# Kernel optimization log

Hardware: AMD Instinct MI355X
Metric: run time of the kernel (lower is better)

The kernel has to match this reference:

```python
import jax, jax.numpy as jnp
import numpy as np

N_DIM = 1024
HEAD_NUM = 16
HEAD_DIM = N_DIM // HEAD_NUM


def setup_inputs() -> dict:
    key = jax.random.key(0)
    ks = jax.random.split(key, 6)
    s = 1.0 / np.sqrt(N_DIM)
    return {
        "x": jax.random.normal(ks[0], (2, 2048, N_DIM), dtype=jnp.float32),
        "wq": jax.random.uniform(ks[1], (N_DIM, N_DIM), jnp.float32, -s, s),
        "wk": jax.random.uniform(ks[2], (N_DIM, N_DIM), jnp.float32, -s, s),
        "wv": jax.random.uniform(ks[3], (N_DIM, N_DIM), jnp.float32, -s, s),
        "wo": jax.random.uniform(ks[4], (N_DIM, N_DIM), jnp.float32, -s, s),
        "bo": jax.random.uniform(ks[5], (N_DIM,), jnp.float32, -s, s),
    }


def reference(x, wq, wk, wv, wo, bo):
    B, S, D = x.shape
    # torch Linear: y = x @ W.T
    def proj(w):
        return (x @ w.T).reshape(B, S, HEAD_NUM, HEAD_DIM).transpose(0, 2, 1, 3)  # [B,H,S,Dh]
    q, k, v = proj(wq), proj(wk), proj(wv)
    scale = 1.0 / np.sqrt(HEAD_DIM).astype(np.float32)
    scores = jnp.einsum("bhqd,bhkd->bhqk", q, k) * scale  # [B,H,S,S]
    attn = jax.nn.softmax(scores, axis=-1)
    y = jnp.einsum("bhqk,bhkd->bhqd", attn, v)  # [B,H,S,Dh]
    y = y.transpose(0, 2, 1, 3).reshape(B, S, D)
    return y @ wo.T + bo
```

## Files before the change

kernel.cpp:

```cpp
#include <hip/hip_runtime.h>
#include <math.h>

#define B_DIM 2
#define S_DIM 2048
#define D_DIM 1024
#define H_NUM 16
#define DH    64
#define M_DIM (B_DIM * S_DIM)

typedef __attribute__((ext_vector_type(8))) short short8;
typedef __attribute__((ext_vector_type(4))) short short4v;
typedef __attribute__((ext_vector_type(4))) float float4v;
typedef __attribute__((ext_vector_type(4))) unsigned short ushort4v;
typedef unsigned short ushort;

static __device__ __forceinline__ ushort f2bf(float f) {
    unsigned u = __float_as_uint(f);
    u += 0x7fffu + ((u >> 16) & 1u);
    return (ushort)(u >> 16);
}

static __device__ __forceinline__ float fexp2(float x) {
#if __has_builtin(__builtin_amdgcn_exp2f)
    return __builtin_amdgcn_exp2f(x);
#else
    return exp2f(x);
#endif
}

static __device__ __forceinline__ unsigned cvtpk_bf16(float lo, float hi) {
    unsigned r;
    asm("v_cvt_pk_bf16_f32 %0, %1, %2" : "=v"(r) : "v"(lo), "v"(hi));
    return r;
}

static __device__ __forceinline__ void gload_lds16(const void* g, void* l) {
    __builtin_amdgcn_global_load_lds(
        (const __attribute__((address_space(1))) void*)g,
        (__attribute__((address_space(3))) void*)l, 16, 0, 0);
}

__global__ __launch_bounds__(256)
void cast_all(const float* __restrict__ x,  const float* __restrict__ wq,
              const float* __restrict__ wk, const float* __restrict__ wv,
              const float* __restrict__ wo, ushort* __restrict__ dst)
{
    const int i = blockIdx.x * 256 + threadIdx.x;
    const float4* s;
    int off;
    if      (i < 1048576) { s = (const float4*)x;  off = 0;       }
    else if (i < 1310720) { s = (const float4*)wq; off = 1048576; }
    else if (i < 1572864) { s = (const float4*)wk; off = 1310720; }
    else if (i < 1835008) { s = (const float4*)wv; off = 1572864; }
    else                  { s = (const float4*)wo; off = 1835008; }
    const float4 v = s[i - off];
    ushort4v o;
    o[0] = f2bf(v.x); o[1] = f2bf(v.y); o[2] = f2bf(v.z); o[3] = f2bf(v.w);
    ((ushort4v*)dst)[i] = o;
}

__global__ __launch_bounds__(256)
void gemm_bf16(const ushort* __restrict__ A, const ushort* __restrict__ B,
               ushort* __restrict__ Qh, ushort* __restrict__ Kh,
               ushort* __restrict__ Vt)
{
    __shared__ ushort Asm[2][128 * 64];
    __shared__ ushort Bsm[2][128 * 64];

    const int K = 1024;
    const int NT = 16;
    const int lin = blockIdx.y * 24 + blockIdx.x;
    const int swz = (lin & 7) * 96 + (lin >> 3);
    const int n0 = (swz % 24) * 128;
    const int m0 = (swz / 24) * 128;
    const int t    = threadIdx.x;
    const int w    = t >> 6;
    const int lane = t & 63;
    const int n    = lane & 15;
    const int quad = lane >> 4;
    const int wm = w >> 1, wn = w & 1;

    const int l8 = lane >> 3;
    const int sg = (lane & 7) ^ l8;

    const int fswz[2] = { ((0 * 4 + quad) ^ (n & 7)) * 8,
                          ((1 * 4 + quad) ^ (n & 7)) * 8 };

    float4v acc[4][4];
#pragma unroll
    for (int mt = 0; mt < 4; ++mt)
#pragma unroll
        for (int nt = 0; nt < 4; ++nt) acc[mt][nt] = (float4v){0.f, 0.f, 0.f, 0.f};

#pragma unroll
    for (int i = 0; i < 4; ++i) {
        gload_lds16(&A[(size_t)(m0 + w * 32 + i * 8 + l8) * K + sg * 8],
                    &Asm[0][(w * 32 + i * 8) * 64]);
        gload_lds16(&B[(size_t)(n0 + w * 32 + i * 8 + l8) * K + sg * 8],
                    &Bsm[0][(w * 32 + i * 8) * 64]);
    }

    for (int kt6 = 0; kt6 < NT; ++kt6) {
        __syncthreads();
        const int cur = kt6 & 1;
        if (kt6 + 1 < NT) {
            const int kt1 = (kt6 + 1) * 64;
            const int nxt = cur ^ 1;
#pragma unroll
            for (int i = 0; i < 4; ++i) {
                gload_lds16(&A[(size_t)(m0 + w * 32 + i * 8 + l8) * K + kt1 + sg * 8],
                            &Asm[nxt][(w * 32 + i * 8) * 64]);
                gload_lds16(&B[(size_t)(n0 + w * 32 + i * 8 + l8) * K + kt1 + sg * 8],
                            &Bsm[nxt][(w * 32 + i * 8) * 64]);
            }
        }

        short8 af[4][2], bfr[4][2];
#pragma unroll
        for (int mt = 0; mt < 4; ++mt)
#pragma unroll
            for (int kk = 0; kk < 2; ++kk)
                af[mt][kk] = *(const short8*)&Asm[cur][(wm * 64 + mt * 16 + n) * 64 + fswz[kk]];
#pragma unroll
        for (int nt = 0; nt < 4; ++nt)
#pragma unroll
            for (int kk = 0; kk < 2; ++kk)
                bfr[nt][kk] = *(const short8*)&Bsm[cur][(wn * 64 + nt * 16 + n) * 64 + fswz[kk]];

        __builtin_amdgcn_s_setprio(1);
#pragma unroll
        for (int mt = 0; mt < 4; ++mt)
#pragma unroll
            for (int nt = 0; nt < 4; ++nt) {
                acc[mt][nt] = __builtin_amdgcn_mfma_f32_16x16x32_bf16(
                    af[mt][0], bfr[nt][0], acc[mt][nt], 0, 0, 0);
                acc[mt][nt] = __builtin_amdgcn_mfma_f32_16x16x32_bf16(
                    af[mt][1], bfr[nt][1], acc[mt][nt], 0, 0, 0);
            }
        __builtin_amdgcn_s_setprio(0);
    }

    const int wid = n0 >> 10;
    ushort* dstQK = (wid == 0) ? Qh : Kh;
    const float qs = (wid == 0) ? 0.1803368801f : 1.0f;
#pragma unroll
    for (int mt = 0; mt < 4; ++mt) {
        const int m = m0 + wm * 64 + mt * 16 + quad * 4;
        const int b = m >> 11, s = m & (S_DIM - 1);
#pragma unroll
        for (int nt = 0; nt < 4; ++nt) {
            const int ng = (n0 & 1023) + wn * 64 + nt * 16 + n;
            const int h = ng >> 6, d = ng & 63;
            const int bh = b * H_NUM + h;
            if (wid < 2) {
#pragma unroll
                for (int r = 0; r < 4; ++r)
                    dstQK[(((size_t)bh * S_DIM + s + r) << 6) + d] =
                        f2bf(acc[mt][nt][r] * qs);
            } else {
                ushort4v p;
#pragma unroll
                for (int r = 0; r < 4; ++r) p[r] = f2bf(acc[mt][nt][r]);
                *(ushort4v*)&Vt[(((size_t)bh * DH + d) << 11) + s] = p;
            }
        }
    }
}

__global__ __launch_bounds__(256)
void gemm_out(const ushort* __restrict__ A, const ushort* __restrict__ B,
              float* __restrict__ Of, const float* __restrict__ bias)
{
    __shared__ ushort Asm[2][128 * 64];
    __shared__ ushort Bsm[2][64 * 64];

    const int K = 1024;
    const int NT = 16;
    const int lin = blockIdx.y * 16 + blockIdx.x;
    const int swz = (lin & 7) * 64 + (lin >> 3);
    const int n0 = (swz % 16) * 64;
    const int m0 = (swz / 16) * 128;
    const int t    = threadIdx.x;
    const int w    = t >> 6;
    const int lane = t & 63;
    const int n    = lane & 15;
    const int quad = lane >> 4;
    const int wm = w >> 1, wn = w & 1;

    const int l8 = lane >> 3;
    const int sg = (lane & 7) ^ l8;
    const int fswz[2] = { ((0 * 4 + quad) ^ (n & 7)) * 8,
                          ((1 * 4 + quad) ^ (n & 7)) * 8 };

    float4v acc[4][2];
#pragma unroll
    for (int mt = 0; mt < 4; ++mt)
#pragma unroll
        for (int nt = 0; nt < 2; ++nt) acc[mt][nt] = (float4v){0.f, 0.f, 0.f, 0.f};

#pragma unroll
    for (int i = 0; i < 4; ++i)
        gload_lds16(&A[(size_t)(m0 + w * 32 + i * 8 + l8) * K + sg * 8],
                    &Asm[0][(w * 32 + i * 8) * 64]);
#pragma unroll
    for (int i = 0; i < 2; ++i)
        gload_lds16(&B[(size_t)(n0 + w * 16 + i * 8 + l8) * K + sg * 8],
                    &Bsm[0][(w * 16 + i * 8) * 64]);

    for (int kt6 = 0; kt6 < NT; ++kt6) {
        __syncthreads();
        const int cur = kt6 & 1;
        if (kt6 + 1 < NT) {
            const int kt1 = (kt6 + 1) * 64;
            const int nxt = cur ^ 1;
#pragma unroll
            for (int i = 0; i < 4; ++i)
                gload_lds16(&A[(size_t)(m0 + w * 32 + i * 8 + l8) * K + kt1 + sg * 8],
                            &Asm[nxt][(w * 32 + i * 8) * 64]);
#pragma unroll
            for (int i = 0; i < 2; ++i)
                gload_lds16(&B[(size_t)(n0 + w * 16 + i * 8 + l8) * K + kt1 + sg * 8],
                            &Bsm[nxt][(w * 16 + i * 8) * 64]);
        }

        short8 af[4][2], bfr[2][2];
#pragma unroll
        for (int mt = 0; mt < 4; ++mt)
#pragma unroll
            for (int kk = 0; kk < 2; ++kk)
                af[mt][kk] = *(const short8*)&Asm[cur][(wm * 64 + mt * 16 + n) * 64 + fswz[kk]];
#pragma unroll
        for (int nt = 0; nt < 2; ++nt)
#pragma unroll
            for (int kk = 0; kk < 2; ++kk)
                bfr[nt][kk] = *(const short8*)&Bsm[cur][(wn * 32 + nt * 16 + n) * 64 + fswz[kk]];

        __builtin_amdgcn_s_setprio(1);
#pragma unroll
        for (int mt = 0; mt < 4; ++mt)
#pragma unroll
            for (int nt = 0; nt < 2; ++nt) {
                acc[mt][nt] = __builtin_amdgcn_mfma_f32_16x16x32_bf16(
                    af[mt][0], bfr[nt][0], acc[mt][nt], 0, 0, 0);
                acc[mt][nt] = __builtin_amdgcn_mfma_f32_16x16x32_bf16(
                    af[mt][1], bfr[nt][1], acc[mt][nt], 0, 0, 0);
            }
        __builtin_amdgcn_s_setprio(0);
    }

#pragma unroll
    for (int mt = 0; mt < 4; ++mt) {
        const int m = m0 + wm * 64 + mt * 16 + quad * 4;
#pragma unroll
        for (int nt = 0; nt < 2; ++nt) {
            const int ng = n0 + wn * 32 + nt * 16 + n;
            const float bv = bias[ng];
#pragma unroll
            for (int r = 0; r < 4; ++r)
                Of[(size_t)(m + r) * D_DIM + ng] = acc[mt][nt][r] + bv;
        }
    }
}

__global__ __launch_bounds__(256)
void attn_mfma(const ushort* __restrict__ Qh, const ushort* __restrict__ Kh,
               const ushort* __restrict__ Vt, ushort* __restrict__ Yh)
{
    __shared__ ushort Ksm[2][64 * 64];
    __shared__ ushort Vsm[2][64 * 64];

    const int w    = threadIdx.x >> 6;
    const int lane = threadIdx.x & 63;
    const int n    = lane & 15;
    const int quad = lane >> 4;

    const int wave_id = blockIdx.x * 4 + w;
    const int bh    = wave_id >> 6;
    const int qbase = (wave_id & 63) * 32;
    const int b     = bh >> 4;
    const int h     = bh & (H_NUM - 1);

    const ushort* Qb = Qh + (((size_t)bh * S_DIM) << 6);
    const ushort* Kb = Kh + (((size_t)bh * S_DIM) << 6);
    const ushort* Vb = Vt + (((size_t)bh * DH) << 11);

    const int l8 = lane >> 3;
    const int sg = (lane & 7) ^ l8;

    short8 qa[2][2];
#pragma unroll
    for (int mt = 0; mt < 2; ++mt)
#pragma unroll
        for (int kc = 0; kc < 2; ++kc)
            qa[mt][kc] = *(const short8*)&Qb[((size_t)(qbase + mt * 16 + n) << 6) + kc * 32 + quad * 8];

    float4v O[2][4];
    float   mrow[2], lrow[2];
#pragma unroll
    for (int mt = 0; mt < 2; ++mt) {
#pragma unroll
        for (int nt = 0; nt < 4; ++nt) O[mt][nt] = (float4v){0.f, 0.f, 0.f, 0.f};
        mrow[mt] = -1e30f; lrow[mt] = 0.f;
    }

    const int fswz[2] = { ((0 * 4 + quad) ^ (n & 7)) * 8,
                          ((1 * 4 + quad) ^ (n & 7)) * 8 };
    const int h4 = (quad & 1) * 4;
    const int q2 = quad >> 1;
    int vswz[2][2];
#pragma unroll
    for (int kc = 0; kc < 2; ++kc)
#pragma unroll
        for (int cc = 0; cc < 2; ++cc)
            vswz[kc][cc] = (((4 * kc + 2 * cc + q2) ^ (n & 7)) << 3) + h4;

#pragma unroll
    for (int i = 0; i < 2; ++i) {
        gload_lds16(&Kb[(size_t)(w * 16 + i * 8 + l8) * 64 + sg * 8],
                    &Ksm[0][(w * 16 + i * 8) * 64]);
        gload_lds16(&Vb[(size_t)(w * 16 + i * 8 + l8) * 2048 + sg * 8],
                    &Vsm[0][(w * 16 + i * 8) * 64]);
    }

    for (int kb = 0; kb < S_DIM / 64; ++kb) {
        __syncthreads();
        const int cur = kb & 1;
        if (kb + 1 < S_DIM / 64) {
            const int key1 = (kb + 1) * 64;
            const int nxt  = cur ^ 1;
#pragma unroll
            for (int i = 0; i < 2; ++i) {
                gload_lds16(&Kb[(size_t)(key1 + w * 16 + i * 8 + l8) * 64 + sg * 8],
                            &Ksm[nxt][(w * 16 + i * 8) * 64]);
                gload_lds16(&Vb[(size_t)(w * 16 + i * 8 + l8) * 2048 + key1 + sg * 8],
                            &Vsm[nxt][(w * 16 + i * 8) * 64]);
            }
        }

        short8 kf[4][2];
#pragma unroll
        for (int ct = 0; ct < 4; ++ct)
#pragma unroll
            for (int kc = 0; kc < 2; ++kc)
                kf[ct][kc] = *(const short8*)&Ksm[cur][(ct * 16 + n) * 64 + fswz[kc]];

        float4v s[2][4];
        __builtin_amdgcn_s_setprio(1);
#pragma unroll
        for (int mt = 0; mt < 2; ++mt)
#pragma unroll
            for (int ct = 0; ct < 4; ++ct) {
                float4v a = (float4v){0.f, 0.f, 0.f, 0.f};
                a = __builtin_amdgcn_mfma_f32_16x16x32_bf16(kf[ct][0], qa[mt][0], a, 0, 0, 0);
                a = __builtin_amdgcn_mfma_f32_16x16x32_bf16(kf[ct][1], qa[mt][1], a, 0, 0, 0);
                s[mt][ct] = a;
            }
        __builtin_amdgcn_s_setprio(0);

        short8 vf[4][2];
#pragma unroll
        for (int nt = 0; nt < 4; ++nt) {
            const int rb = (nt * 16 + n) * 64;
#pragma unroll
            for (int kc = 0; kc < 2; ++kc) {
                const short4v g0 = *(const short4v*)&Vsm[cur][rb + vswz[kc][0]];
                const short4v g1 = *(const short4v*)&Vsm[cur][rb + vswz[kc][1]];
                vf[nt][kc] = __builtin_shufflevector(g0, g1, 0, 1, 2, 3, 4, 5, 6, 7);
            }
        }

#pragma unroll
        for (int mt = 0; mt < 2; ++mt) {
            float lm = s[mt][0][0];
#pragma unroll
            for (int ct = 0; ct < 4; ++ct)
#pragma unroll
                for (int r = 0; r < 4; ++r)
                    lm = fmaxf(lm, s[mt][ct][r]);
            lm = fmaxf(lm, __shfl_xor(lm, 16, 64));
            lm = fmaxf(lm, __shfl_xor(lm, 32, 64));

            const bool ev = lm > mrow[mt] + 8.0f;
            if (__any(ev)) {
                const float mnew  = ev ? lm : mrow[mt];
                const float alpha = fexp2(mrow[mt] - mnew);
                mrow[mt] = mnew;
                lrow[mt] *= alpha;
                const int ai = __float_as_int(alpha);
                float av[4];
#pragma unroll
                for (int r = 0; r < 4; ++r)
                    av[r] = __int_as_float(
                        __builtin_amdgcn_ds_bpermute(4 * (quad * 4 + r), ai));
#pragma unroll
                for (int nt = 0; nt < 4; ++nt)
#pragma unroll
                    for (int r = 0; r < 4; ++r) O[mt][nt][r] *= av[r];
            }

            float pv[4][4];
            float lsum = 0.f;
#pragma unroll
            for (int ct = 0; ct < 4; ++ct)
#pragma unroll
                for (int r = 0; r < 4; ++r) {
                    const float p = fexp2(s[mt][ct][r] - mrow[mt]);
                    pv[ct][r] = p;
                    lsum += p;
                }
            lrow[mt] += lsum;

            union { unsigned u[4]; short8 s8; } pk[2];
#pragma unroll
            for (int kc = 0; kc < 2; ++kc) {
                pk[kc].u[0] = cvtpk_bf16(pv[2 * kc][0],     pv[2 * kc][1]);
                pk[kc].u[1] = cvtpk_bf16(pv[2 * kc][2],     pv[2 * kc][3]);
                pk[kc].u[2] = cvtpk_bf16(pv[2 * kc + 1][0], pv[2 * kc + 1][1]);
                pk[kc].u[3] = cvtpk_bf16(pv[2 * kc + 1][2], pv[2 * kc + 1][3]);
            }

            __builtin_amdgcn_s_setprio(1);
#pragma unroll
            for (int nt = 0; nt < 4; ++nt) {
                O[mt][nt] = __builtin_amdgcn_mfma_f32_16x16x32_bf16(pk[0].s8, vf[nt][0], O[mt][nt], 0, 0, 0);
                O[mt][nt] = __builtin_amdgcn_mfma_f32_16x16x32_bf16(pk[1].s8, vf[nt][1], O[mt][nt], 0, 0, 0);
            }
            __builtin_amdgcn_s_setprio(0);
        }
    }

#pragma unroll
    for (int mt = 0; mt < 2; ++mt) {
        float ls = lrow[mt];
        ls += __shfl_xor(ls, 16, 64);
        ls += __shfl_xor(ls, 32, 64);
        const float linv = 1.f / ls;
        const int  li = __float_as_int(linv);
        float lv[4];
#pragma unroll
        for (int r = 0; r < 4; ++r)
            lv[r] = __int_as_float(
                __builtin_amdgcn_ds_bpermute(4 * (quad * 4 + r), li));
#pragma unroll
        for (int nt = 0; nt < 4; ++nt)
#pragma unroll
            for (int r = 0; r < 4; ++r) {
                const int q = qbase + mt * 16 + quad * 4 + r;
                Yh[((size_t)(b * S_DIM + q) << 10) + h * DH + nt * 16 + n] =
                    f2bf(O[mt][nt][r] * lv[r]);
            }
    }
}

extern "C" void kernel_launch(void* const* d_in, const int* in_sizes, int n_in,
                              void* d_out, int out_size, void* d_ws, size_t ws_size,
                              hipStream_t stream)
{
    const float* x  = (const float*)d_in[0];
    const float* wq = (const float*)d_in[1];
    const float* wk = (const float*)d_in[2];
    const float* wv = (const float*)d_in[3];
    const float* wo = (const float*)d_in[4];
    const float* bo = (const float*)d_in[5];
    float* out = (float*)d_out;

    const size_t MD = (size_t)M_DIM * D_DIM;
    const size_t WD = (size_t)D_DIM * D_DIM;
    ushort* xh  = (ushort*)d_ws;
    ushort* Wh  = xh + MD;
    ushort* Woh = Wh + 3 * WD;
    ushort* Qh  = Woh + WD;
    ushort* Kh  = Qh + MD;
    ushort* Vt  = Kh + MD;
    ushort* Yh  = Vt + MD;
    if (ws_size < 48u * 1024u * 1024u) return;

    dim3 blk(256);
    cast_all<<<dim3(8192), blk, 0, stream>>>(x, wq, wk, wv, wo, xh);

    gemm_bf16<<<dim3(24, 32), blk, 0, stream>>>(xh, Wh, Qh, Kh, Vt);
    attn_mfma<<<dim3(512), blk, 0, stream>>>(Qh, Kh, Vt, Yh);
    gemm_out<<<dim3(16, 32), blk, 0, stream>>>(Yh, Woh, out, bo);
}
```

Baseline: 202.8 us.

## Split attention over the key dimension with a separate merge kernel

Splits the attention key loop into two halves run as separate blocks (grid y = 2). Each half writes unnormalized fp32 partial outputs plus row max and sum to workspace, and a new merge kernel combines them with log-sum-exp rescaling into bf16 Y. The goal is more blocks in flight on the MI355X's many CUs, which the original 512-block grid leaves underused. The cost is about 32 MB of extra fp32 traffic, an additional kernel launch, and reliance on a workspace of at least 81 MB, with the old path kept as a fallback.

```diff
diff --git a/kernel.cpp b/kernel.cpp
--- a/kernel.cpp
+++ b/kernel.cpp
@@ -264,7 +264,9 @@
 
 __global__ __launch_bounds__(256)
 void attn_mfma(const ushort* __restrict__ Qh, const ushort* __restrict__ Kh,
-               const ushort* __restrict__ Vt, ushort* __restrict__ Yh)
+               const ushort* __restrict__ Vt, ushort* __restrict__ Yh,
+               float* __restrict__ Op, float* __restrict__ Lm,
+               int nkb, int partial)
 {
     __shared__ ushort Ksm[2][64 * 64];
     __shared__ ushort Vsm[2][64 * 64];
@@ -279,6 +281,8 @@
     const int qbase = (wave_id & 63) * 32;
     const int b     = bh >> 4;
     const int h     = bh & (H_NUM - 1);
+    const int s     = blockIdx.y;
+    const int kb0   = s * nkb, kb1 = kb0 + nkb;
 
     const ushort* Qb = Qh + (((size_t)bh * S_DIM) << 6);
     const ushort* Kb = Kh + (((size_t)bh * S_DIM) << 6);
@@ -314,18 +318,19 @@
         for (int cc = 0; cc < 2; ++cc)
             vswz[kc][cc] = (((4 * kc + 2 * cc + q2) ^ (n & 7)) << 3) + h4;
 
+    const int keyp = kb0 * 64;
 #pragma unroll
     for (int i = 0; i < 2; ++i) {
-        gload_lds16(&Kb[(size_t)(w * 16 + i * 8 + l8) * 64 + sg * 8],
+        gload_lds16(&Kb[(size_t)(keyp + w * 16 + i * 8 + l8) * 64 + sg * 8],
                     &Ksm[0][(w * 16 + i * 8) * 64]);
-        gload_lds16(&Vb[(size_t)(w * 16 + i * 8 + l8) * 2048 + sg * 8],
+        gload_lds16(&Vb[(size_t)(w * 16 + i * 8 + l8) * 2048 + keyp + sg * 8],
                     &Vsm[0][(w * 16 + i * 8) * 64]);
     }
 
-    for (int kb = 0; kb < S_DIM / 64; ++kb) {
+    for (int kb = kb0; kb < kb1; ++kb) {
         __syncthreads();
-        const int cur = kb & 1;
-        if (kb + 1 < S_DIM / 64) {
+        const int cur = (kb - kb0) & 1;
+        if (kb + 1 < kb1) {
             const int key1 = (kb + 1) * 64;
             const int nxt  = cur ^ 1;
 #pragma unroll
@@ -344,7 +349,7 @@
             for (int kc = 0; kc < 2; ++kc)
                 kf[ct][kc] = *(const short8*)&Ksm[cur][(ct * 16 + n) * 64 + fswz[kc]];
 
-        float4v s[2][4];
+        float4v sc[2][4];
         __builtin_amdgcn_s_setprio(1);
 #pragma unroll
         for (int mt = 0; mt < 2; ++mt)
@@ -353,7 +358,7 @@
                 float4v a = (float4v){0.f, 0.f, 0.f, 0.f};
                 a = __builtin_amdgcn_mfma_f32_16x16x32_bf16(kf[ct][0], qa[mt][0], a, 0, 0, 0);
                 a = __builtin_amdgcn_mfma_f32_16x16x32_bf16(kf[ct][1], qa[mt][1], a, 0, 0, 0);
-                s[mt][ct] = a;
+                sc[mt][ct] = a;
             }
         __builtin_amdgcn_s_setprio(0);
 
@@ -371,12 +376,12 @@
 
 #pragma unroll
         for (int mt = 0; mt < 2; ++mt) {
-            float lm = s[mt][0][0];
+            float lm = sc[mt][0][0];
 #pragma unroll
             for (int ct = 0; ct < 4; ++ct)
 #pragma unroll
                 for (int r = 0; r < 4; ++r)
-                    lm = fmaxf(lm, s[mt][ct][r]);
+                    lm = fmaxf(lm, sc[mt][ct][r]);
             lm = fmaxf(lm, __shfl_xor(lm, 16, 64));
             lm = fmaxf(lm, __shfl_xor(lm, 32, 64));
 
@@ -404,7 +409,7 @@
             for (int ct = 0; ct < 4; ++ct)
 #pragma unroll
                 for (int r = 0; r < 4; ++r) {
-                    const float p = fexp2(s[mt][ct][r] - mrow[mt]);
+                    const float p = fexp2(sc[mt][ct][r] - mrow[mt]);
                     pv[ct][r] = p;
                     lsum += p;
                 }
@@ -429,27 +434,77 @@
         }
     }
 
-#pragma unroll
-    for (int mt = 0; mt < 2; ++mt) {
-        float ls = lrow[mt];
-        ls += __shfl_xor(ls, 16, 64);
-        ls += __shfl_xor(ls, 32, 64);
-        const float linv = 1.f / ls;
-        const int  li = __float_as_int(linv);
-        float lv[4];
-#pragma unroll
-        for (int r = 0; r < 4; ++r)
-            lv[r] = __int_as_float(
-                __builtin_amdgcn_ds_bpermute(4 * (quad * 4 + r), li));
-#pragma unroll
-        for (int nt = 0; nt < 4; ++nt)
+    if (!partial) {
+#pragma unroll
+        for (int mt = 0; mt < 2; ++mt) {
+            float ls = lrow[mt];
+            ls += __shfl_xor(ls, 16, 64);
+            ls += __shfl_xor(ls, 32, 64);
+            const float linv = 1.f / ls;
+            const int  li = __float_as_int(linv);
+            float lv[4];
+#pragma unroll
+            for (int r = 0; r < 4; ++r)
+                lv[r] = __int_as_float(
+                    __builtin_amdgcn_ds_bpermute(4 * (quad * 4 + r), li));
+#pragma unroll
+            for (int nt = 0; nt < 4; ++nt)
+#pragma unroll
+                for (int r = 0; r < 4; ++r) {
+                    const int q = qbase + mt * 16 + quad * 4 + r;
+                    Yh[((size_t)(b * S_DIM + q) << 10) + h * DH + nt * 16 + n] =
+                        f2bf(O[mt][nt][r] * lv[r]);
+                }
+        }
+    } else {
+        float* Ops = Op + (size_t)s * ((size_t)M_DIM * 1024);
+        float* Lms = Lm + (size_t)s * (32 * S_DIM * 2);
+#pragma unroll
+        for (int mt = 0; mt < 2; ++mt) {
+            float ls = lrow[mt];
+            ls += __shfl_xor(ls, 16, 64);
+            ls += __shfl_xor(ls, 32, 64);
+            if (quad == 0) {
+                const int q = qbase + mt * 16 + n;
+                Lms[((size_t)bh * S_DIM + q) * 2 + 0] = mrow[mt];
+                Lms[((size_t)bh * S_DIM + q) * 2 + 1] = ls;
+            }
 #pragma unroll
             for (int r = 0; r < 4; ++r) {
                 const int q = qbase + mt * 16 + quad * 4 + r;
-                Yh[((size_t)(b * S_DIM + q) << 10) + h * DH + nt * 16 + n] =
-                    f2bf(O[mt][nt][r] * lv[r]);
-            }
-    }
+                const size_t base = ((size_t)bh * S_DIM + q) * DH;
+#pragma unroll
+                for (int nt = 0; nt < 4; ++nt)
+                    Ops[base + nt * 16 + n] = O[mt][nt][r];
+            }
+        }
+    }
+}
+
+__global__ __launch_bounds__(256)
+void attn_merge(const float* __restrict__ Op, const float* __restrict__ Lm,
+                ushort* __restrict__ Yh)
+{
+    const int idx = blockIdx.x * 256 + threadIdx.x;
+    const int d4 = idx & 15;
+    const int q  = (idx >> 4) & (S_DIM - 1);
+    const int bh = idx >> 15;
+    const size_t po = ((size_t)bh * S_DIM + q) * DH + d4 * 4;
+    const float4 o0 = *(const float4*)(Op + po);
+    const float4 o1 = *(const float4*)(Op + (size_t)M_DIM * 1024 + po);
+    const size_t li = ((size_t)bh * S_DIM + q) * 2;
+    const float m0 = Lm[li],              l0 = Lm[li + 1];
+    const float m1 = Lm[32 * S_DIM * 2 + li], l1 = Lm[32 * S_DIM * 2 + li + 1];
+    const float mm = fmaxf(m0, m1);
+    const float a0 = fexp2(m0 - mm), a1 = fexp2(m1 - mm);
+    const float linv = 1.f / (l0 * a0 + l1 * a1);
+    ushort4v y;
+    y[0] = f2bf((o0.x * a0 + o1.x * a1) * linv);
+    y[1] = f2bf((o0.y * a0 + o1.y * a1) * linv);
+    y[2] = f2bf((o0.z * a0 + o1.z * a1) * linv);
+    y[3] = f2bf((o0.w * a0 + o1.w * a1) * linv);
+    const int b = bh >> 4, h = bh & (H_NUM - 1);
+    *(ushort4v*)&Yh[((size_t)(b * S_DIM + q) << 10) + h * DH + d4 * 4] = y;
 }
 
 extern "C" void kernel_launch(void* const* d_in, const int* in_sizes, int n_in,
@@ -473,12 +528,20 @@
     ushort* Kh  = Qh + MD;
     ushort* Vt  = Kh + MD;
     ushort* Yh  = Vt + MD;
+    float*  Op  = (float*)(Yh + MD);
+    float*  Lm  = Op + 2 * MD;
     if (ws_size < 48u * 1024u * 1024u) return;
+    const bool split = ws_size >= 81u * 1024u * 1024u;
 
     dim3 blk(256);
     cast_all<<<dim3(8192), blk, 0, stream>>>(x, wq, wk, wv, wo, xh);
 
     gemm_bf16<<<dim3(24, 32), blk, 0, stream>>>(xh, Wh, Qh, Kh, Vt);
-    attn_mfma<<<dim3(512), blk, 0, stream>>>(Qh, Kh, Vt, Yh);
+    if (split) {
+        attn_mfma<<<dim3(512, 2), blk, 0, stream>>>(Qh, Kh, Vt, nullptr, Op, Lm, 16, 1);
+        attn_merge<<<dim3(4096), blk, 0, stream>>>(Op, Lm, Yh);
+    } else {
+        attn_mfma<<<dim3(512, 1), blk, 0, stream>>>(Qh, Kh, Vt, Yh, nullptr, nullptr, 32, 0);
+    }
     gemm_out<<<dim3(16, 32), blk, 0, stream>>>(Yh, Woh, out, bo);
 }
```

After: 215.0 us. 1.06x slower.
